# Kernel optimization log

Measured on AMD Instinct MI355X. Metric: run time of the kernel, lower is better.

Reference implementation:

```python
import jax, jax.numpy as jnp
import numpy as np

HID = 64


def setup_inputs() -> dict:
    key = jax.random.key(0)
    k = jax.random.split(key, 7)
    B, T = 4096, 8192
    x = jax.random.normal(k[0], (B, T, 1), dtype=jnp.float32)
    # Kaiming-uniform-ish init scale; exact values irrelevant for correctness baseline
    W_in = jax.random.normal(k[1], (1, HID), dtype=jnp.float32) * 0.5
    b_in = jax.random.normal(k[2], (HID,), dtype=jnp.float32) * 0.1
    W_s = jax.random.normal(k[3], (HID, HID), dtype=jnp.float32) * (1.0 / np.sqrt(HID))
    b_s = jax.random.normal(k[4], (HID,), dtype=jnp.float32) * 0.1
    W_out = jax.random.normal(k[5], (HID, 1), dtype=jnp.float32) * (1.0 / np.sqrt(HID))
    b_out = jax.random.normal(k[6], (1,), dtype=jnp.float32) * 0.1
    return {"x": x, "W_in": W_in, "b_in": b_in, "W_s": W_s, "b_s": b_s,
            "W_out": W_out, "b_out": b_out}


def reference(x, W_in, b_in, W_s, b_s, W_out, b_out):
    B, T, _ = x.shape
    xt = jnp.swapaxes(x, 0, 1)  # [T, B, 1] -> scan over time

    def step(h, x_t):
        # input_proj on [B,1] -> [B,HID]; tiny GEMM per step (the recurrence is sequential)
        inp = x_t @ W_in + b_in
        h = jax.nn.gelu(h @ W_s + b_s + inp, approximate=False)  # torch GELU = exact erf
        return h, None

    h0 = jnp.zeros((B, HID), dtype=x.dtype)
    h_final, _ = jax.lax.scan(step, h0, xt)
    return h_final @ W_out + b_out  # [B, 1]
```

## Files before the change

kernel.cpp:

```cpp
#include <hip/hip_runtime.h>
#include <cstdint>
#include <cstddef>

#define HID 64
#define RPG 16
#define HSTR 72

typedef short bf16x8 __attribute__((ext_vector_type(8)));
typedef float f32x4 __attribute__((ext_vector_type(4)));

__device__ __forceinline__ float fast_gelu(float z) {
    float u = z * 0.70710678118654752f;
    float a = __builtin_fabsf(u);
    float t = __builtin_amdgcn_rcpf(__builtin_fmaf(0.3275911f, a, 1.0f));
    float e = __builtin_amdgcn_exp2f((u * u) * -1.44269504088896f);
    float p =                   1.061405429f;
    p = __builtin_fmaf(p, t, -1.453152027f);
    p = __builtin_fmaf(p, t,  1.421413741f);
    p = __builtin_fmaf(p, t, -0.284496736f);
    p = __builtin_fmaf(p, t,  0.254829592f);
    p = p * t;
    float er = __builtin_fmaf(-p, e, 1.0f);
    er = __builtin_copysignf(er, u);
    float zh = 0.5f * z;
    return __builtin_fmaf(zh, er, zh);
}

__device__ __forceinline__ ushort bf16_hi(float f) {
    return (ushort)(__float_as_uint(f) >> 16);
}
__device__ __forceinline__ float bf16_f(ushort u) {
    return __uint_as_float(((unsigned)u) << 16);
}

__global__ __launch_bounds__(256, 1)
void ssm_kernel(const float* __restrict__ x,
                const float* __restrict__ W_in,
                const float* __restrict__ b_in,
                const float* __restrict__ W_s,
                const float* __restrict__ b_s,
                const float* __restrict__ W_out,
                const float* __restrict__ b_out,
                float* __restrict__ out,
                int B, int T) {
    __shared__ ushort hlds[2][2][RPG * HSTR];
    __shared__ float  xlds[64][RPG];

    const int tid  = threadIdx.x;
    const int wv   = tid >> 6;
    const int lane = tid & 63;
    const int q    = lane >> 4;
    const int rr   = lane & 15;
    const int bA   = blockIdx.x * RPG;
    const int c    = (wv << 4) | rr;

    bf16x8 Bhi[2], Blo[2];
#pragma unroll
    for (int half = 0; half < 2; ++half) {
#pragma unroll
        for (int e = 0; e < 8; ++e) {
            const int k = half * 32 + q * 8 + e;
            const float wf = W_s[k * HID + c];
            const ushort hi = bf16_hi(wf);
            const float lof = wf - bf16_f(hi);
            Bhi[half][e] = (short)hi;
            Blo[half][e] = (short)bf16_hi(lof);
        }
    }

    const float win = W_in[c];
    const float cb  = b_in[c] + b_s[c];

    {
        ushort* p = &hlds[0][0][0];
        for (int i = tid; i < 2 * RPG * HSTR; i += 256) p[i] = 0;
    }

    const int nch = T >> 6;
    int pp = 0;

    for (int tc = 0; tc < nch; ++tc) {
        {
            const int t4 = (wv << 4) + (q << 2);
            const float4 xg = *reinterpret_cast<const float4*>(
                &x[(size_t)(bA + rr) * (size_t)T + (size_t)(tc * 64 + t4)]);
            xlds[t4 + 0][rr] = xg.x;
            xlds[t4 + 1][rr] = xg.y;
            xlds[t4 + 2][rr] = xg.z;
            xlds[t4 + 3][rr] = xg.w;
        }
        __syncthreads();

#pragma unroll 2
        for (int tl = 0; tl < 64; ++tl) {
            const int np = pp ^ 1;
            const f32x4 xr = *reinterpret_cast<const f32x4*>(&xlds[tl][q << 2]);
            f32x4 acc1;
#pragma unroll
            for (int e = 0; e < 4; ++e) acc1[e] = __builtin_fmaf(xr[e], win, cb);
            f32x4 acc2 = {0.f, 0.f, 0.f, 0.f};

            const ushort* hp = &hlds[pp][0][0];
            const ushort* lp = &hlds[pp][1][0];
            const int aoff = rr * HSTR + (q << 3);
            const bf16x8 Ahi0 = *reinterpret_cast<const bf16x8*>(hp + aoff);
            const bf16x8 Ahi1 = *reinterpret_cast<const bf16x8*>(hp + aoff + 32);
            const bf16x8 Alo0 = *reinterpret_cast<const bf16x8*>(lp + aoff);
            const bf16x8 Alo1 = *reinterpret_cast<const bf16x8*>(lp + aoff + 32);

            acc1 = __builtin_amdgcn_mfma_f32_16x16x32_bf16(Ahi0, Bhi[0], acc1, 0, 0, 0);
            acc1 = __builtin_amdgcn_mfma_f32_16x16x32_bf16(Ahi1, Bhi[1], acc1, 0, 0, 0);
            acc2 = __builtin_amdgcn_mfma_f32_16x16x32_bf16(Ahi0, Blo[0], acc2, 0, 0, 0);
            acc2 = __builtin_amdgcn_mfma_f32_16x16x32_bf16(Ahi1, Blo[1], acc2, 0, 0, 0);
            acc2 = __builtin_amdgcn_mfma_f32_16x16x32_bf16(Alo0, Bhi[0], acc2, 0, 0, 0);
            acc2 = __builtin_amdgcn_mfma_f32_16x16x32_bf16(Alo1, Bhi[1], acc2, 0, 0, 0);

            ushort* whp = &hlds[np][0][0];
            ushort* wlp = &hlds[np][1][0];
#pragma unroll
            for (int e = 0; e < 4; ++e) {
                const float z = acc1[e] + acc2[e];
                const float h = fast_gelu(z);
                const unsigned hb = __float_as_uint(h);
                const float lof = h - __uint_as_float(hb & 0xffff0000u);
                const int widx = ((q << 2) + e) * HSTR + c;
                whp[widx] = (ushort)(hb >> 16);
                wlp[widx] = bf16_hi(lof);
            }
            __syncthreads();
            pp ^= 1;
        }
    }

    {
        const int row = (wv << 2) + q;
        const int c4  = rr << 2;
        const ushort* hp = &hlds[pp][0][row * HSTR + c4];
        const ushort* lp = &hlds[pp][1][row * HSTR + c4];
        float s = 0.f;
#pragma unroll
        for (int j = 0; j < 4; ++j) {
            const float hv = bf16_f(hp[j]) + bf16_f(lp[j]);
            s = __builtin_fmaf(hv, W_out[c4 + j], s);
        }
        s += __shfl_xor(s, 1, 64);
        s += __shfl_xor(s, 2, 64);
        s += __shfl_xor(s, 4, 64);
        s += __shfl_xor(s, 8, 64);
        if (rr == 0) out[bA + row] = s + b_out[0];
    }
}

extern "C" void kernel_launch(void* const* d_in, const int* in_sizes, int n_in,
                              void* d_out, int out_size, void* d_ws, size_t ws_size,
                              hipStream_t stream) {
    const float* x     = (const float*)d_in[0];
    const float* W_in  = (const float*)d_in[1];
    const float* b_in  = (const float*)d_in[2];
    const float* W_s   = (const float*)d_in[3];
    const float* b_s   = (const float*)d_in[4];
    const float* W_out = (const float*)d_in[5];
    const float* b_out = (const float*)d_in[6];
    float* out = (float*)d_out;

    const int B = out_size;
    const int T = in_sizes[0] / B;

    const int blocks = B / RPG;
    ssm_kernel<<<blocks, 256, 0, stream>>>(
        x, W_in, b_in, W_s, b_s, W_out, b_out, out, B, T);
}
```

Before: 3.147 ms.

## Split GELU epilogue across two wave groups per block with 512 threads

Doubles the block to 8 waves. Each pair of waves computes the same MFMA tile redundantly, and each wave handles two of the four output rows in the GELU and split-bf16 writeback, which halves the per-wave serial epilogue on the recurrence's critical path. The MFMA chains are restructured into three independent accumulators to shorten dependency latency, and the x chunk load is changed to coalesced scalar loads. The cost is duplicated MFMA work, larger barriers across 8 waves, and higher register pressure under launch_bounds(512,2).

```diff
diff --git a/kernel.cpp b/kernel.cpp
--- a/kernel.cpp
+++ b/kernel.cpp
@@ -8,6 +8,7 @@
 
 typedef short bf16x8 __attribute__((ext_vector_type(8)));
 typedef float f32x4 __attribute__((ext_vector_type(4)));
+typedef float f32x2 __attribute__((ext_vector_type(2)));
 
 __device__ __forceinline__ float fast_gelu(float z) {
     float u = z * 0.70710678118654752f;
@@ -33,7 +34,47 @@
     return __uint_as_float(((unsigned)u) << 16);
 }
 
-__global__ __launch_bounds__(256, 1)
+#define STEP(RHI, RLO, WHI, WLO, E0, E1) { \
+    const bf16x8 Ahi0 = *reinterpret_cast<const bf16x8*>(RHI); \
+    const bf16x8 Ahi1 = *reinterpret_cast<const bf16x8*>((RHI) + 32); \
+    const bf16x8 Alo0 = *reinterpret_cast<const bf16x8*>(RLO); \
+    const bf16x8 Alo1 = *reinterpret_cast<const bf16x8*>((RLO) + 32); \
+    const f32x2 xr = *reinterpret_cast<const f32x2*>(&xlds[tl][4 * q + E0]); \
+    const f32x4 zz = {0.f, 0.f, 0.f, 0.f}; \
+    f32x4 ahh = __builtin_amdgcn_mfma_f32_16x16x32_bf16(Ahi0, Bhi0, zz, 0, 0, 0); \
+    f32x4 ac1 = __builtin_amdgcn_mfma_f32_16x16x32_bf16(Ahi0, Blo0, zz, 0, 0, 0); \
+    f32x4 ac2 = __builtin_amdgcn_mfma_f32_16x16x32_bf16(Alo0, Bhi0, zz, 0, 0, 0); \
+    ahh = __builtin_amdgcn_mfma_f32_16x16x32_bf16(Ahi1, Bhi1, ahh, 0, 0, 0); \
+    ac1 = __builtin_amdgcn_mfma_f32_16x16x32_bf16(Ahi1, Blo1, ac1, 0, 0, 0); \
+    ac2 = __builtin_amdgcn_mfma_f32_16x16x32_bf16(Alo1, Bhi1, ac2, 0, 0, 0); \
+    const float z0 = (ahh[E0] + ac1[E0]) + (ac2[E0] + __builtin_fmaf(xr[0], win, cb)); \
+    const float z1 = (ahh[E1] + ac1[E1]) + (ac2[E1] + __builtin_fmaf(xr[1], win, cb)); \
+    const float h0 = fast_gelu(z0); \
+    const float h1 = fast_gelu(z1); \
+    const unsigned hb0 = __float_as_uint(h0), hb1 = __float_as_uint(h1); \
+    (WHI)[0]    = (ushort)(hb0 >> 16); \
+    (WHI)[HSTR] = (ushort)(hb1 >> 16); \
+    (WLO)[0]    = bf16_hi(h0 - __uint_as_float(hb0 & 0xffff0000u)); \
+    (WLO)[HSTR] = bf16_hi(h1 - __uint_as_float(hb1 & 0xffff0000u)); \
+    __syncthreads(); }
+
+#define MAINLOOP(E0, E1) { \
+    ushort* const whi1 = &hlds[1][0][(4 * q + E0) * HSTR + c]; \
+    ushort* const wlo1 = &hlds[1][1][(4 * q + E0) * HSTR + c]; \
+    ushort* const whi0 = &hlds[0][0][(4 * q + E0) * HSTR + c]; \
+    ushort* const wlo0 = &hlds[0][1][(4 * q + E0) * HSTR + c]; \
+    for (int tc = 0; tc < nch; ++tc) { \
+        xlds[lane][ww]     = x[(size_t)(bA + ww) * (size_t)T + (size_t)(tc * 64) + lane]; \
+        xlds[lane][ww + 8] = x[(size_t)(bA + ww + 8) * (size_t)T + (size_t)(tc * 64) + lane]; \
+        __syncthreads(); \
+        _Pragma("unroll 1") \
+        for (int tl2 = 0; tl2 < 32; ++tl2) { \
+            { const int tl = 2 * tl2;     STEP(rhi0, rlo0, whi1, wlo1, E0, E1) } \
+            { const int tl = 2 * tl2 + 1; STEP(rhi1, rlo1, whi0, wlo0, E0, E1) } \
+        } \
+    } }
+
+__global__ __launch_bounds__(512, 2)
 void ssm_kernel(const float* __restrict__ x,
                 const float* __restrict__ W_in,
                 const float* __restrict__ b_in,
@@ -47,96 +88,57 @@
     __shared__ float  xlds[64][RPG];
 
     const int tid  = threadIdx.x;
-    const int wv   = tid >> 6;
+    const int ww   = tid >> 6;
+    const int g    = ww & 3;
+    const int hf   = ww >> 2;
     const int lane = tid & 63;
     const int q    = lane >> 4;
     const int rr   = lane & 15;
     const int bA   = blockIdx.x * RPG;
-    const int c    = (wv << 4) | rr;
+    const int c    = (g << 4) | rr;
 
-    bf16x8 Bhi[2], Blo[2];
+    if (bA >= B) return;
+
+    bf16x8 Bhi0, Bhi1, Blo0, Blo1;
 #pragma unroll
-    for (int half = 0; half < 2; ++half) {
-#pragma unroll
-        for (int e = 0; e < 8; ++e) {
-            const int k = half * 32 + q * 8 + e;
-            const float wf = W_s[k * HID + c];
+    for (int e = 0; e < 8; ++e) {
+        {
+            const float wf = W_s[(q * 8 + e) * HID + c];
             const ushort hi = bf16_hi(wf);
-            const float lof = wf - bf16_f(hi);
-            Bhi[half][e] = (short)hi;
-            Blo[half][e] = (short)bf16_hi(lof);
+            Bhi0[e] = (short)hi;
+            Blo0[e] = (short)bf16_hi(wf - bf16_f(hi));
+        }
+        {
+            const float wf = W_s[(32 + q * 8 + e) * HID + c];
+            const ushort hi = bf16_hi(wf);
+            Bhi1[e] = (short)hi;
+            Blo1[e] = (short)bf16_hi(wf - bf16_f(hi));
         }
     }
+    asm volatile("" : "+v"(Bhi0), "+v"(Bhi1), "+v"(Blo0), "+v"(Blo1));
 
     const float win = W_in[c];
     const float cb  = b_in[c] + b_s[c];
 
     {
         ushort* p = &hlds[0][0][0];
-        for (int i = tid; i < 2 * RPG * HSTR; i += 256) p[i] = 0;
+        for (int i = tid; i < 2 * RPG * HSTR; i += 512) p[i] = 0;
     }
 
+    const ushort* const rhi0 = &hlds[0][0][rr * HSTR + q * 8];
+    const ushort* const rlo0 = &hlds[0][1][rr * HSTR + q * 8];
+    const ushort* const rhi1 = &hlds[1][0][rr * HSTR + q * 8];
+    const ushort* const rlo1 = &hlds[1][1][rr * HSTR + q * 8];
+
     const int nch = T >> 6;
-    int pp = 0;
 
-    for (int tc = 0; tc < nch; ++tc) {
-        {
-            const int t4 = (wv << 4) + (q << 2);
-            const float4 xg = *reinterpret_cast<const float4*>(
-                &x[(size_t)(bA + rr) * (size_t)T + (size_t)(tc * 64 + t4)]);
-            xlds[t4 + 0][rr] = xg.x;
-            xlds[t4 + 1][rr] = xg.y;
-            xlds[t4 + 2][rr] = xg.z;
-            xlds[t4 + 3][rr] = xg.w;
-        }
-        __syncthreads();
+    if (hf == 0) { MAINLOOP(0, 1) } else { MAINLOOP(2, 3) }
 
-#pragma unroll 2
-        for (int tl = 0; tl < 64; ++tl) {
-            const int np = pp ^ 1;
-            const f32x4 xr = *reinterpret_cast<const f32x4*>(&xlds[tl][q << 2]);
-            f32x4 acc1;
-#pragma unroll
-            for (int e = 0; e < 4; ++e) acc1[e] = __builtin_fmaf(xr[e], win, cb);
-            f32x4 acc2 = {0.f, 0.f, 0.f, 0.f};
-
-            const ushort* hp = &hlds[pp][0][0];
-            const ushort* lp = &hlds[pp][1][0];
-            const int aoff = rr * HSTR + (q << 3);
-            const bf16x8 Ahi0 = *reinterpret_cast<const bf16x8*>(hp + aoff);
-            const bf16x8 Ahi1 = *reinterpret_cast<const bf16x8*>(hp + aoff + 32);
-            const bf16x8 Alo0 = *reinterpret_cast<const bf16x8*>(lp + aoff);
-            const bf16x8 Alo1 = *reinterpret_cast<const bf16x8*>(lp + aoff + 32);
-
-            acc1 = __builtin_amdgcn_mfma_f32_16x16x32_bf16(Ahi0, Bhi[0], acc1, 0, 0, 0);
-            acc1 = __builtin_amdgcn_mfma_f32_16x16x32_bf16(Ahi1, Bhi[1], acc1, 0, 0, 0);
-            acc2 = __builtin_amdgcn_mfma_f32_16x16x32_bf16(Ahi0, Blo[0], acc2, 0, 0, 0);
-            acc2 = __builtin_amdgcn_mfma_f32_16x16x32_bf16(Ahi1, Blo[1], acc2, 0, 0, 0);
-            acc2 = __builtin_amdgcn_mfma_f32_16x16x32_bf16(Alo0, Bhi[0], acc2, 0, 0, 0);
-            acc2 = __builtin_amdgcn_mfma_f32_16x16x32_bf16(Alo1, Bhi[1], acc2, 0, 0, 0);
-
-            ushort* whp = &hlds[np][0][0];
-            ushort* wlp = &hlds[np][1][0];
-#pragma unroll
-            for (int e = 0; e < 4; ++e) {
-                const float z = acc1[e] + acc2[e];
-                const float h = fast_gelu(z);
-                const unsigned hb = __float_as_uint(h);
-                const float lof = h - __uint_as_float(hb & 0xffff0000u);
-                const int widx = ((q << 2) + e) * HSTR + c;
-                whp[widx] = (ushort)(hb >> 16);
-                wlp[widx] = bf16_hi(lof);
-            }
-            __syncthreads();
-            pp ^= 1;
-        }
-    }
-
-    {
-        const int row = (wv << 2) + q;
+    if (hf == 0) {
+        const int row = (g << 2) + q;
         const int c4  = rr << 2;
-        const ushort* hp = &hlds[pp][0][row * HSTR + c4];
-        const ushort* lp = &hlds[pp][1][row * HSTR + c4];
+        const ushort* hp = &hlds[0][0][row * HSTR + c4];
+        const ushort* lp = &hlds[0][1][row * HSTR + c4];
         float s = 0.f;
 #pragma unroll
         for (int j = 0; j < 4; ++j) {
@@ -167,6 +169,6 @@
     const int T = in_sizes[0] / B;
 
     const int blocks = B / RPG;
-    ssm_kernel<<<blocks, 256, 0, stream>>>(
+    ssm_kernel<<<blocks, 512, 0, stream>>>(
         x, W_in, b_in, W_s, b_s, W_out, b_out, out, B, T);
 }
```

Result: faster. 2.817 ms (-10.5%).
